# Optimization experiments

Measured on AMD Instinct MI355X. Metric: run time of the kernel, lower is better.

The kernel has to match this reference:

```python
import jax, jax.numpy as jnp
import numpy as np
from functools import partial

PAD, SOD = 1, 2
VOCAB, E, H = 32000, 512, 512
BSZ, DOCLEN, SENTLEN, SRCLEN = 8, 16, 40, 400
MAXPOS = 62  # max_target_positions + 2
NEG = -1e9


def setup_inputs() -> dict:
    key = jax.random.key(0)
    ks = jax.random.split(key, 16)
    s = 0.05  # weight scale for numerical sanity
    emb = jax.random.normal(ks[0], (VOCAB, E), jnp.float32) * 0.1
    emb = emb.at[PAD].set(0.0)
    spe = jax.random.normal(ks[1], (MAXPOS, E), jnp.float32) * 0.1
    spe = spe.at[PAD].set(0.0)
    return {
        'prev_output_tokens': jax.random.randint(ks[2], (BSZ, DOCLEN, SENTLEN), 0, VOCAB),
        'encoder_out0': jax.random.normal(ks[3], (BSZ, SRCLEN, H), jnp.float32),
        'encoder_out1': jax.random.normal(ks[4], (BSZ, SRCLEN, H), jnp.float32),
        'encoder_padding_mask': jnp.zeros((BSZ, SRCLEN), bool),
        'embed_tokens': emb,
        'sent_pos_emb': spe,
        'w_ih_doc': jax.random.normal(ks[5], (4 * H, E), jnp.float32) * s,
        'w_hh_doc': jax.random.normal(ks[6], (4 * H, H), jnp.float32) * s,
        'b_ih_doc': jnp.zeros((4 * H,), jnp.float32),
        'b_hh_doc': jnp.zeros((4 * H,), jnp.float32),
        'attn_q_doc': jax.random.normal(ks[7], (H, H), jnp.float32) * s,
        'attn_o_doc': jax.random.normal(ks[8], (H, 2 * H), jnp.float32) * s,
        'w_ih_w': jax.random.normal(ks[9], (4 * H, E), jnp.float32) * s,
        'w_hh_w': jax.random.normal(ks[10], (4 * H, H), jnp.float32) * s,
        'b_ih_w': jnp.zeros((4 * H,), jnp.float32),
        'b_hh_w': jnp.zeros((4 * H,), jnp.float32),
        'attn_q_w': jax.random.normal(ks[11], (H, H), jnp.float32) * s,
        'attn_o_w': jax.random.normal(ks[12], (H, 2 * H), jnp.float32) * s,
        'fc_out_w': jax.random.normal(ks[13], (VOCAB, H), jnp.float32) * s,
        'fc_out_b': jnp.zeros((VOCAB,), jnp.float32),
    }


def _lstm_cell(x, h, c, w_ih, w_hh, b_ih, b_hh):
    g = x @ w_ih.T + h @ w_hh.T + b_ih + b_hh
    i, f, gg, o = jnp.split(g, 4, axis=-1)
    c = jax.nn.sigmoid(f) * c + jax.nn.sigmoid(i) * jnp.tanh(gg)
    h = jax.nn.sigmoid(o) * jnp.tanh(c)
    return h, c


def _attend(h, src, mask, wq, wo):
    # fairseq-style additive-bilinear attention: score = <src, Wq h>
    q = h @ wq.T                                  # [b, d]
    s = jnp.einsum('bsd,bd->bs', src, q)          # [b, srclen]
    s = jnp.where(mask, NEG, s)
    p = jax.nn.softmax(s, axis=-1)
    ctx = jnp.einsum('bs,bsd->bd', p, src)
    out = jnp.tanh(jnp.concatenate([ctx, h], axis=-1) @ wo.T)
    return out, p


def reference(prev_output_tokens, encoder_out0, encoder_out1, encoder_padding_mask,
              embed_tokens, sent_pos_emb,
              w_ih_doc, w_hh_doc, b_ih_doc, b_hh_doc, attn_q_doc, attn_o_doc,
              w_ih_w, w_hh_w, b_ih_w, b_hh_w, attn_q_w, attn_o_w,
              fc_out_w, fc_out_b):
    bsz, doclen, sentlen = prev_output_tokens.shape
    srclen = encoder_out0.shape[1]

    # ---- document-level LSTM + attention loop (one step per sentence) ----
    h0 = encoder_out0.mean(axis=1)                 # src_summary_h0
    x0 = jnp.broadcast_to(embed_tokens[SOD], (bsz, E))

    def doc_step(carry, _):
        h, c, inp = carry
        h, c = _lstm_cell(inp, h, c, w_ih_doc, w_hh_doc, b_ih_doc, b_hh_doc)
        out, _p = _attend(h, encoder_out0, encoder_padding_mask, attn_q_doc, attn_o_doc)
        return (h, c, out), out

    (_, _, last_out), doc_outs = jax.lax.scan(doc_step, (h0, h0, x0), None, length=doclen)
    sent_states = doc_outs.transpose(1, 0, 2).reshape(bsz * doclen, H)

    # ---- sentence positions (make_sent_positions) ----
    nonempty = (prev_output_tokens != PAD).sum(axis=2) != 0     # [bsz, doclen]
    pos = jnp.where(nonempty, PAD + 1 + jnp.arange(doclen), 1)
    sp = sent_pos_emb[pos.reshape(bsz * doclen)]                # [B2, E]

    # ---- word-level decoder over flattened sentences ----
    B2 = bsz * doclen
    ys = prev_output_tokens.reshape(B2, sentlen)
    x_in = embed_tokens[ys] + sp[:, None, :]                    # [B2, S, E]
    enc_w = jnp.repeat(encoder_out1, doclen, axis=0)            # [B2, srclen, d]
    mask_w = jnp.repeat(encoder_padding_mask, doclen, axis=0)

    def word_step(carry, x_t):
        h, c = carry
        h, c = _lstm_cell(x_t, h, c, w_ih_w, w_hh_w, b_ih_w, b_hh_w)
        out, p = _attend(h, enc_w, mask_w, attn_q_w, attn_o_w)
        return (h, c), (out, p)

    (_, _), (w_outs, w_scores) = jax.lax.scan(
        word_step, (sent_states, sent_states), x_in.transpose(1, 0, 2))
    w_outs = w_outs.transpose(1, 0, 2)                          # [B2, S, H]
    word_atte_scores = w_scores.transpose(1, 0, 2)              # [B2, S, srclen]

    logits = jnp.einsum('bsh,vh->bsv', w_outs, fc_out_w) + fc_out_b
    dec_outs = logits.reshape(bsz, doclen * sentlen, VOCAB)

    attn_scores = jnp.zeros((bsz, doclen, srclen), dec_outs.dtype)  # zeros as in original
    return dec_outs, attn_scores, word_atte_scores, last_out
```

## Files before the change

### kernel.cpp

```cpp
#include <hip/hip_runtime.h>
#include <cstdint>

typedef unsigned short u16;
typedef unsigned int u32;
typedef __attribute__((ext_vector_type(8))) short bf16x8;
typedef __attribute__((ext_vector_type(8))) unsigned short u16x8;
typedef __attribute__((ext_vector_type(4))) float f32x4;

struct us4 { u16 a, b, c, d; };

__device__ __forceinline__ u16 f2bf(float f) {
    uint32_t u = __float_as_uint(f);
    uint32_t r = (u + 0x7FFFu + ((u >> 16) & 1u)) >> 16;
    return (u16)r;
}
__device__ __forceinline__ float bf2f(u16 h) { return __uint_as_float(((uint32_t)h) << 16); }
__device__ __forceinline__ float sigm(float x) { return 1.f / (1.f + expf(-x)); }
__device__ __forceinline__ float dot4(float4 a, float4 b) {
    return a.x * b.x + a.y * b.y + a.z * b.z + a.w * b.w;
}
__device__ __forceinline__ float wave_sum(float v) {
#pragma unroll
    for (int o = 32; o; o >>= 1) v += __shfl_down(v, o);
    return v;
}
__device__ __forceinline__ float wave_max(float v) {
#pragma unroll
    for (int o = 32; o; o >>= 1) v = fmaxf(v, __shfl_down(v, o));
    return v;
}

__device__ __forceinline__ void ast(u32* p, u32 v) {
    __hip_atomic_store(p, v, __ATOMIC_RELAXED, __HIP_MEMORY_SCOPE_AGENT);
}
__device__ __forceinline__ u32 ald(const u32* p) {
    return __hip_atomic_load(p, __ATOMIC_RELAXED, __HIP_MEMORY_SCOPE_AGENT);
}
__device__ __forceinline__ u32 packsplit(float v) {
    u16 h = f2bf(v);
    u16 l = f2bf(v - bf2f(h));
    return (u32)h | ((u32)l << 16);
}

template <int NBLK>
__device__ __forceinline__ void fbar(u32* flags, int me, u32 gen) {
    asm volatile("s_waitcnt vmcnt(0)" ::: "memory");
    __syncthreads();
    if (threadIdx.x == 0) ast(&flags[me * 32], gen);
    if (threadIdx.x < NBLK) {
        while (ald(&flags[threadIdx.x * 32]) < gen)
            __builtin_amdgcn_s_sleep(1);
    }
    __syncthreads();
    asm volatile("" ::: "memory");
}

template <bool SPLIT, int AMODE, int EPI, int XMAJ = 0>
__global__ __launch_bounds__(256) void gemm_bt(
    const u16* __restrict__ AH, const u16* __restrict__ AL, int lda, long strideA,
    const u16* __restrict__ BH, const u16* __restrict__ BL, int ldb, long strideB,
    float* __restrict__ C, u16* __restrict__ CH, u16* __restrict__ CL,
    int ldc, long strideC, const float* __restrict__ bias, int K)
{
    constexpr int TL = 40;
    constexpr int CHK = 128 * TL;
    __shared__ u16 sm[(SPLIT ? 4 : 2) * CHK];
    u16* sAH = sm;
    u16* sBH = sm + CHK;
    u16* sAL = SPLIT ? sm + 2 * CHK : sm;
    u16* sBL = SPLIT ? sm + 3 * CHK : sm;

    const int tid = threadIdx.x;
    const int lane = tid & 63, w = tid >> 6;
    const int wm = w >> 1, wn = w & 1;
    const int lane15 = lane & 15, q8 = (lane >> 4) << 3;
    const int n0 = (XMAJ ? blockIdx.y : blockIdx.x) * 128;
    const int m0 = (XMAJ ? blockIdx.x : blockIdx.y) * 128;
    const int z = blockIdx.z;

    const int r = tid >> 2, c8 = (tid & 3) * 8;

    long aoff[2], boff[2];
#pragma unroll
    for (int h2 = 0; h2 < 2; ++h2) {
        int row = r + (h2 << 6);
        if (AMODE == 0) {
            aoff[h2] = strideA * z + (long)(m0 + row) * lda + c8;
        } else {
            int m = m0 + row;
            int t = m % 40, dd = m / 40;
            aoff[h2] = ((long)(t + 1) * 128 + (z * 16 + dd)) * 512 + c8;
        }
        boff[h2] = strideB * z + (long)(n0 + row) * ldb + c8;
    }

    f32x4 acc[4][4] = {};

    for (int k0 = 0; k0 < K; k0 += 32) {
#pragma unroll
        for (int h2 = 0; h2 < 2; ++h2) {
            int row = r + (h2 << 6);
            int sidx = row * TL + c8;
            *(u16x8*)&sAH[sidx] = *(const u16x8*)&AH[aoff[h2] + k0];
            *(u16x8*)&sBH[sidx] = *(const u16x8*)&BH[boff[h2] + k0];
            if constexpr (SPLIT) {
                *(u16x8*)&sAL[sidx] = *(const u16x8*)&AL[aoff[h2] + k0];
                *(u16x8*)&sBL[sidx] = *(const u16x8*)&BL[boff[h2] + k0];
            }
        }
        __syncthreads();

        bf16x8 a[4], b[4], al[4], bl[4];
#pragma unroll
        for (int i = 0; i < 4; ++i) {
            a[i] = *(const bf16x8*)&sAH[(wm * 64 + i * 16 + lane15) * TL + q8];
            b[i] = *(const bf16x8*)&sBH[(wn * 64 + i * 16 + lane15) * TL + q8];
            if constexpr (SPLIT) {
                al[i] = *(const bf16x8*)&sAL[(wm * 64 + i * 16 + lane15) * TL + q8];
                bl[i] = *(const bf16x8*)&sBL[(wn * 64 + i * 16 + lane15) * TL + q8];
            }
        }
#pragma unroll
        for (int mt = 0; mt < 4; ++mt)
#pragma unroll
            for (int nt = 0; nt < 4; ++nt) {
                acc[mt][nt] = __builtin_amdgcn_mfma_f32_16x16x32_bf16(a[mt], b[nt], acc[mt][nt], 0, 0, 0);
                if constexpr (SPLIT) {
                    acc[mt][nt] = __builtin_amdgcn_mfma_f32_16x16x32_bf16(a[mt], bl[nt], acc[mt][nt], 0, 0, 0);
                    acc[mt][nt] = __builtin_amdgcn_mfma_f32_16x16x32_bf16(al[mt], b[nt], acc[mt][nt], 0, 0, 0);
                }
            }
        __syncthreads();
    }

#pragma unroll
    for (int mt = 0; mt < 4; ++mt)
#pragma unroll
        for (int nt = 0; nt < 4; ++nt)
#pragma unroll
            for (int i = 0; i < 4; ++i) {
                int row = m0 + wm * 64 + mt * 16 + ((lane >> 4) << 2) + i;
                int col = n0 + wn * 64 + nt * 16 + lane15;
                long off = strideC * z + (long)row * ldc + col;
                float v = acc[mt][nt][i];
                if constexpr (EPI == 0) {
                    C[off] = v;
                } else if constexpr (EPI == 1) {
                    C[off] = v + bias[col];
                } else if constexpr (EPI == 2) {
                    u16 h_ = f2bf(v);
                    CH[off] = h_;
                    CL[off] = f2bf(v - bf2f(h_));
                } else if constexpr (EPI == 3) {
                    CH[off] = f2bf(tanhf(v));
                } else {
                    CH[off] = f2bf(v);
                }
            }
}

__global__ __launch_bounds__(256) void gemm_head(
    const u16* __restrict__ enc1H, const u16* __restrict__ enc1L,
    const u16* __restrict__ wqTH,  const u16* __restrict__ wqTL,
    const u16* __restrict__ enc0H, const u16* __restrict__ enc0L,
    const u16* __restrict__ wqdTH, const u16* __restrict__ wqdTL,
    const u16* __restrict__ woCH,  const u16* __restrict__ woCL,
    const u16* __restrict__ xinH,  const u16* __restrict__ xinL,
    const u16* __restrict__ WihH,  const u16* __restrict__ WihL,
    u16* __restrict__ sq1H, u16* __restrict__ sq1L,
    float* __restrict__ E0q, float* __restrict__ E0o,
    float* __restrict__ xW, const float* __restrict__ biasc)
{
    constexpr int TL = 40;
    constexpr int CHK = 128 * TL;
    __shared__ u16 sm[4 * CHK];
    u16* sAH = sm;
    u16* sBH = sm + CHK;
    u16* sAL = sm + 2 * CHK;
    u16* sBL = sm + 3 * CHK;

    const int bid = blockIdx.x;
    const u16 *AH, *AL, *BH, *BL;
    int task, n0, m0, ldc;
    if (bid < 300) {
        task = bid / 100;
        int rr = bid % 100;
        n0 = (rr & 3) * 128; m0 = (rr >> 2) * 128; ldc = 512;
        if (task == 0)      { AH = enc1H; AL = enc1L; BH = wqTH;  BL = wqTL;  }
        else if (task == 1) { AH = enc0H; AL = enc0L; BH = wqdTH; BL = wqdTL; }
        else                { AH = enc0H; AL = enc0L; BH = woCH;  BL = woCL;  }
    } else {
        task = 3;
        int rr = bid - 300;
        n0 = (rr & 15) * 128; m0 = (rr >> 4) * 128; ldc = 2048;
        AH = xinH; AL = xinL; BH = WihH; BL = WihL;
    }

    const int tid = threadIdx.x;
    const int lane = tid & 63, w = tid >> 6;
    const int wm = w >> 1, wn = w & 1;
    const int lane15 = lane & 15, q8 = (lane >> 4) << 3;
    const int r = tid >> 2, c8 = (tid & 3) * 8;

    long aoff[2], boff[2];
#pragma unroll
    for (int h2 = 0; h2 < 2; ++h2) {
        int row = r + (h2 << 6);
        aoff[h2] = (long)(m0 + row) * 512 + c8;
        boff[h2] = (long)(n0 + row) * 512 + c8;
    }

    f32x4 acc[4][4] = {};
    for (int k0 = 0; k0 < 512; k0 += 32) {
#pragma unroll
        for (int h2 = 0; h2 < 2; ++h2) {
            int row = r + (h2 << 6);
            int sidx = row * TL + c8;
            *(u16x8*)&sAH[sidx] = *(const u16x8*)&AH[aoff[h2] + k0];
            *(u16x8*)&sBH[sidx] = *(const u16x8*)&BH[boff[h2] + k0];
            *(u16x8*)&sAL[sidx] = *(const u16x8*)&AL[aoff[h2] + k0];
            *(u16x8*)&sBL[sidx] = *(const u16x8*)&BL[boff[h2] + k0];
        }
        __syncthreads();
        bf16x8 a[4], b[4], al[4], bl[4];
#pragma unroll
        for (int i = 0; i < 4; ++i) {
            a[i]  = *(const bf16x8*)&sAH[(wm * 64 + i * 16 + lane15) * TL + q8];
            b[i]  = *(const bf16x8*)&sBH[(wn * 64 + i * 16 + lane15) * TL + q8];
            al[i] = *(const bf16x8*)&sAL[(wm * 64 + i * 16 + lane15) * TL + q8];
            bl[i] = *(const bf16x8*)&sBL[(wn * 64 + i * 16 + lane15) * TL + q8];
        }
#pragma unroll
        for (int mt = 0; mt < 4; ++mt)
#pragma unroll
            for (int nt = 0; nt < 4; ++nt) {
                acc[mt][nt] = __builtin_amdgcn_mfma_f32_16x16x32_bf16(a[mt],  b[nt],  acc[mt][nt], 0, 0, 0);
                acc[mt][nt] = __builtin_amdgcn_mfma_f32_16x16x32_bf16(a[mt],  bl[nt], acc[mt][nt], 0, 0, 0);
                acc[mt][nt] = __builtin_amdgcn_mfma_f32_16x16x32_bf16(al[mt], b[nt],  acc[mt][nt], 0, 0, 0);
            }
        __syncthreads();
    }

#pragma unroll
    for (int mt = 0; mt < 4; ++mt)
#pragma unroll
        for (int nt = 0; nt < 4; ++nt)
#pragma unroll
            for (int i = 0; i < 4; ++i) {
                int row = m0 + wm * 64 + mt * 16 + ((lane >> 4) << 2) + i;
                int col = n0 + wn * 64 + nt * 16 + lane15;
                long off = (long)row * ldc + col;
                float v = acc[mt][nt][i];
                if (task == 0) {
                    u16 h_ = f2bf(v);
                    sq1H[off] = h_;
                    sq1L[off] = f2bf(v - bf2f(h_));
                } else if (task == 1) {
                    E0q[off] = v;
                } else if (task == 2) {
                    E0o[off] = v;
                } else {
                    xW[off] = v + biasc[col];
                }
            }
}

#define GLOAD_LDS16(gsrc, ldst) \
    __builtin_amdgcn_global_load_lds((const __attribute__((address_space(1))) u32*)(gsrc), \
                                     (__attribute__((address_space(3))) u32*)(ldst), 16, 0, 0)

__global__ __launch_bounds__(256) void gemm_lds_bias(
    const u16* __restrict__ A, const u16* __restrict__ B,
    float* __restrict__ C, const float* __restrict__ bias, int ldc, int K)
{
    __shared__ u16 sA[128 * 32];
    __shared__ u16 sB[128 * 32];

    const int tid = threadIdx.x;
    const int lane = tid & 63, w = tid >> 6;
    const int wm = w >> 1, wn = w & 1;
    const int lane15 = lane & 15, q8 = (lane >> 4) << 3;
    const int m0 = blockIdx.x * 128;
    const int n0 = blockIdx.y * 128;

    const int srow = lane >> 2, schunk = (lane & 3) * 8;

    f32x4 acc[4][4] = {};

    for (int k0 = 0; k0 < K; k0 += 32) {
#pragma unroll
        for (int c = 0; c < 2; ++c) {
            int base_r = (w * 2 + c) * 16;
            const u16* ga = A + (long)(m0 + base_r + srow) * 512 + k0 + schunk;
            const u16* gb = B + (long)(n0 + base_r + srow) * 512 + k0 + schunk;
            GLOAD_LDS16(ga, &sA[base_r * 32]);
            GLOAD_LDS16(gb, &sB[base_r * 32]);
        }
        __syncthreads();

        bf16x8 a[4], b[4];
#pragma unroll
        for (int i = 0; i < 4; ++i) {
            a[i] = *(const bf16x8*)&sA[(wm * 64 + i * 16 + lane15) * 32 + q8];
            b[i] = *(const bf16x8*)&sB[(wn * 64 + i * 16 + lane15) * 32 + q8];
        }
#pragma unroll
        for (int mt = 0; mt < 4; ++mt)
#pragma unroll
            for (int nt = 0; nt < 4; ++nt)
                acc[mt][nt] = __builtin_amdgcn_mfma_f32_16x16x32_bf16(a[mt], b[nt], acc[mt][nt], 0, 0, 0);
        __syncthreads();
    }

#pragma unroll
    for (int mt = 0; mt < 4; ++mt)
#pragma unroll
        for (int nt = 0; nt < 4; ++nt)
#pragma unroll
            for (int i = 0; i < 4; ++i) {
                int row = m0 + wm * 64 + mt * 16 + ((lane >> 4) << 2) + i;
                int col = n0 + wn * 64 + nt * 16 + lane15;
                __builtin_nontemporal_store(acc[mt][nt][i] + bias[col], &C[(long)row * ldc + col]);
            }
}

__global__ __launch_bounds__(256) void doc_mega(
    const float* __restrict__ enc0, const float* __restrict__ E0q,
    const float* __restrict__ E0o, const unsigned char* __restrict__ mask,
    const float* __restrict__ emb,
    const u16* __restrict__ WpH, const u16* __restrict__ WpL,
    const float* __restrict__ biasd, const float* __restrict__ wo_d,
    u32* __restrict__ dxP, u32* __restrict__ hP0, u32* __restrict__ hP1,
    u32* __restrict__ dcP, u32* __restrict__ dscP,
    float* __restrict__ dsent, float* __restrict__ out_last, u32* bar)
{
    __shared__ u16 xhH[16 * 1032];
    __shared__ u16 xhL[16 * 1032];
    __shared__ float red4[4][16 * 17];
    __shared__ float aux2[512];
    __shared__ float sc_s[512];
    __shared__ float whoh_s[32];
    __shared__ float ctxp[8][32];
    __shared__ float rtmp[8];

    const int blk = blockIdx.x, tid = threadIdx.x;
    const int w = tid >> 6, lane = tid & 63;
    const int b_ = blk >> 4, s = blk & 15;
    const int lane15 = lane & 15, q8 = (lane >> 4) << 3;
    u32* fF = bar;
    u32* fG = bar + 4096 + b_ * 512;
    u32 genF = 0, genG = 0;

    for (int q = tid; q < 8 * 1032; q += 256) { xhH[8 * 1032 + q] = 0; xhL[8 * 1032 + q] = 0; }

    {
        int dd = tid & 31, part = tid >> 5;
        const float* p0 = enc0 + ((long)b_ * 400 + part * 50) * 512 + s * 32 + dd;
        float sm = 0.f;
#pragma unroll 10
        for (int j = 0; j < 50; ++j) { sm += *p0; p0 += 512; }
        ctxp[part][dd] = sm;
        __syncthreads();
        if (tid < 32) {
            float m = 0.f;
#pragma unroll
            for (int p = 0; p < 8; ++p) m += ctxp[p][tid];
            m *= (1.f / 400.f);
            int e = s * 32 + tid;
            ast(&hP0[b_ * 512 + e], packsplit(m));
            ast(&dcP[b_ * 512 + e], __float_as_uint(m));
            ast(&dxP[b_ * 512 + e], packsplit(emb[1024 + e]));
        }
    }
    fbar<128>(fF, blk, ++genF);

    const int eb_b = tid & 7, eb_u4 = tid >> 3, eb_u = blk * 4 + eb_u4;
    float dcr = 0.f;
    if (tid < 32) dcr = __uint_as_float(ald(&dcP[eb_b * 512 + eb_u]));

    const u16* bh_base = WpH + ((long)blk * 16 + lane15) * 1024 + (w << 8) + q8;
    const u16* bl_base = WpL + ((long)blk * 16 + lane15) * 1024 + (w << 8) + q8;
    const u16* ah_base = xhH + lane15 * 1032 + (w << 8) + q8;
    const u16* al_base = xhL + lane15 * 1032 + (w << 8) + q8;

    for (int t = 0; t < 16; ++t) {
        u32* hinP = (t & 1) ? hP1 : hP0;
        u32* houtP = (t & 1) ? hP0 : hP1;

#pragma unroll
        for (int half = 0; half < 2; ++half) {
            u32 px[8], ph[8];
#pragma unroll
            for (int j = 0; j < 8; ++j) {
                int q = half * 2048 + j * 256 + tid;
                px[j] = ald(&dxP[q]);
                ph[j] = ald(&hinP[q]);
            }
#pragma unroll
            for (int j = 0; j < 8; ++j) {
                int q = half * 2048 + j * 256 + tid;
                int o = (q >> 9) * 1032 + (q & 511);
                xhH[o] = (u16)px[j];           xhL[o] = (u16)(px[j] >> 16);
                xhH[o + 512] = (u16)ph[j];     xhL[o + 512] = (u16)(ph[j] >> 16);
            }
        }
        __syncthreads();

        f32x4 acc = {};
#pragma unroll
        for (int k0 = 0; k0 < 256; k0 += 32) {
            bf16x8 aH = *(const bf16x8*)&ah_base[k0];
            bf16x8 aL = *(const bf16x8*)&al_base[k0];
            bf16x8 bH = *(const bf16x8*)&bh_base[k0];
            bf16x8 bL = *(const bf16x8*)&bl_base[k0];
            acc = __builtin_amdgcn_mfma_f32_16x16x32_bf16(aH, bH, acc, 0, 0, 0);
            acc = __builtin_amdgcn_mfma_f32_16x16x32_bf16(aH, bL, acc, 0, 0, 0);
            acc = __builtin_amdgcn_mfma_f32_16x16x32_bf16(aL, bH, acc, 0, 0, 0);
        }
#pragma unroll
        for (int i = 0; i < 4; ++i)
            red4[w][((lane >> 4) * 4 + i) * 17 + lane15] = acc[i];
        __syncthreads();

        if (tid < 32) {
            float g4[4];
#pragma unroll
            for (int g = 0; g < 4; ++g)
                g4[g] = red4[0][eb_b * 17 + eb_u4 * 4 + g] + red4[1][eb_b * 17 + eb_u4 * 4 + g]
                      + red4[2][eb_b * 17 + eb_u4 * 4 + g] + red4[3][eb_b * 17 + eb_u4 * 4 + g];
            float gi = g4[0] + biasd[eb_u];
            float gf = g4[1] + biasd[512 + eb_u];
            float gg = g4[2] + biasd[1024 + eb_u];
            float go = g4[3] + biasd[1536 + eb_u];
            dcr = sigm(gf) * dcr + sigm(gi) * tanhf(gg);
            float hv = sigm(go) * tanhf(dcr);
            ast(&houtP[eb_b * 512 + eb_u], packsplit(hv));
        }
        fbar<128>(fF, blk, ++genF);

        {
            u32 p0 = ald(&houtP[b_ * 512 + tid]);
            u32 p1 = ald(&houtP[b_ * 512 + 256 + tid]);
            aux2[tid] = bf2f((u16)p0) + bf2f((u16)(p0 >> 16));
            aux2[256 + tid] = bf2f((u16)p1) + bf2f((u16)(p1 >> 16));
            __syncthreads();
            for (int jj = w; jj < 25; jj += 4) {
                int j = s * 25 + jj;
                const float4* er = (const float4*)(E0q + ((long)b_ * 400 + j) * 512) + lane * 2;
                const float4* hv = (const float4*)aux2 + lane * 2;
                float sv = dot4(er[0], hv[0]) + dot4(er[1], hv[1]);
                sv = wave_sum(sv);
                if (lane == 0)
                    ast(&dscP[b_ * 400 + j], __float_as_uint(mask[b_ * 400 + j] ? -1e9f : sv));
            }
#pragma unroll
            for (int r = 0; r < 8; ++r) {
                int d = s * 32 + w * 8 + r;
                const float4* wr = (const float4*)(wo_d + (long)d * 1024 + 512) + lane * 2;
                const float4* hv = (const float4*)aux2 + lane * 2;
                float sv = dot4(wr[0], hv[0]) + dot4(wr[1], hv[1]);
                sv = wave_sum(sv);
                if (lane == 0) whoh_s[w * 8 + r] = sv;
            }
        }
        fbar<16>(fG, s, ++genG);

        {
            float v0 = __uint_as_float(ald(&dscP[b_ * 400 + tid]));
            bool h1 = (tid + 256) < 400;
            float v1 = h1 ? __uint_as_float(ald(&dscP[b_ * 400 + tid + 256])) : -1e30f;
            float mx = wave_max(fmaxf(v0, v1));
            if (lane == 0) rtmp[w] = mx;
            __syncthreads();
            float M = fmaxf(fmaxf(rtmp[0], rtmp[1]), fmaxf(rtmp[2], rtmp[3]));
            float e0 = expf(v0 - M);
            float e1 = h1 ? expf(v1 - M) : 0.f;
            float sv = wave_sum(e0 + e1);
            if (lane == 0) rtmp[4 + w] = sv;
            __syncthreads();
            float inv = 1.f / (rtmp[4] + rtmp[5] + rtmp[6] + rtmp[7]);
            sc_s[tid] = e0 * inv;
            if (h1) sc_s[tid + 256] = e1 * inv;
            __syncthreads();
            int dd = tid & 31, part = tid >> 5;
            const float* eo = E0o + ((long)b_ * 400 + part * 50) * 512 + s * 32 + dd;
            float acc2 = 0.f;
#pragma unroll 10
            for (int j = 0; j < 50; ++j) { acc2 += sc_s[part * 50 + j] * (*eo); eo += 512; }
            ctxp[part][dd] = acc2;
            __syncthreads();
            if (tid < 32) {
                int d = s * 32 + tid;
                float o = whoh_s[tid];
#pragma unroll
                for (int p = 0; p < 8; ++p) o += ctxp[p][tid];
                float val = tanhf(o);
                ast(&dxP[b_ * 512 + d], packsplit(val));
                dsent[((b_ << 4) + t) * 512 + d] = val;
                if (t == 15) out_last[b_ * 512 + d] = val;
            }
        }
        fbar<128>(fF, blk, ++genF);
    }
}

__global__ __launch_bounds__(512) void word_mega(
    const float* __restrict__ sentS,
    u32* __restrict__ hAllP,
    u16* __restrict__ hAllH, u16* __restrict__ hAllL,
    const u16* __restrict__ WhhH, const u16* __restrict__ WhhL,
    const float* __restrict__ xW,
    u16* __restrict__ catB, u32* bar)
{
    __shared__ float red[8][4][256];
    const int tid = threadIdx.x, blk = blockIdx.x;
    const int b2t = blk >> 5;
    const int u0 = (blk & 31) << 4;
    u32* fG = bar + 8192 + b2t * 1024;
    u32 genG = 0;

    float wcr = 0.f;
    long cidx = 0;
    int my_b2 = 0, my_u = 0;
    if (tid < 256) {
        my_b2 = b2t * 16 + (tid >> 4);
        my_u = u0 + (tid & 15);
        cidx = (long)my_b2 * 512 + my_u;
        wcr = sentS[cidx];
        ast(&hAllP[cidx], packsplit(wcr));
    }
    fbar<32>(fG, blk & 31, ++genG);

    const int w = tid >> 6, lane = tid & 63;
    const int lane15 = lane & 15, q8 = (lane >> 4) << 3;
    const long arowE = (long)(b2t * 16 + lane15) * 512 + w * 64 + q8;
    long brow[4];
#pragma unroll
    for (int g = 0; g < 4; ++g)
        brow[g] = (long)(g * 512 + u0 + lane15) * 512 + w * 64 + q8;

    for (int t = 0; t < 40; ++t) {
        const u32* hP = hAllP + (long)t * 65536;

        u32 ph[16];
#pragma unroll
        for (int j = 0; j < 16; ++j)
            ph[j] = ald(&hP[arowE + (j >> 3) * 32 + (j & 7)]);

        float xw0 = 0.f, xw1 = 0.f, xw2 = 0.f, xw3 = 0.f;
        if (tid < 256) {
            const float* xr = xW + (long)t * 262144 + (long)my_b2 * 2048;
            xw0 = xr[my_u]; xw1 = xr[512 + my_u]; xw2 = xr[1024 + my_u]; xw3 = xr[1536 + my_u];
        }

        f32x4 acc[4] = {};
#pragma unroll
        for (int half = 0; half < 2; ++half) {
            int k0 = half * 32;
            bf16x8 aH, aL;
#pragma unroll
            for (int j = 0; j < 8; ++j) {
                u32 p = ph[half * 8 + j];
                aH[j] = (short)(p & 0xffffu);
                aL[j] = (short)(p >> 16);
            }
#pragma unroll
            for (int g = 0; g < 4; ++g) {
                bf16x8 bH = *(const bf16x8*)&WhhH[brow[g] + k0];
                bf16x8 bL = *(const bf16x8*)&WhhL[brow[g] + k0];
                acc[g] = __builtin_amdgcn_mfma_f32_16x16x32_bf16(aH, bH, acc[g], 0, 0, 0);
                acc[g] = __builtin_amdgcn_mfma_f32_16x16x32_bf16(aH, bL, acc[g], 0, 0, 0);
                acc[g] = __builtin_amdgcn_mfma_f32_16x16x32_bf16(aL, bH, acc[g], 0, 0, 0);
            }
        }
#pragma unroll
        for (int g = 0; g < 4; ++g)
#pragma unroll
            for (int i = 0; i < 4; ++i)
                red[w][g][((lane >> 4) * 4 + i) * 16 + lane15] = acc[g][i];
        __syncthreads();

        if (tid < 256) {
            float g4[4] = {0.f, 0.f, 0.f, 0.f};
#pragma unroll
            for (int ks = 0; ks < 8; ++ks)
#pragma unroll
                for (int g = 0; g < 4; ++g)
                    g4[g] += red[ks][g][tid];
            float gi = g4[0] + xw0;
            float gf = g4[1] + xw1;
            float gg = g4[2] + xw2;
            float go = g4[3] + xw3;
            wcr = sigm(gf) * wcr + sigm(gi) * tanhf(gg);
            float hv = sigm(go) * tanhf(wcr);
            u16 hh = f2bf(hv);
            u16 ll = f2bf(hv - bf2f(hh));
            long o = (long)(t + 1) * 65536 + cidx;
            ast(&hAllP[o], (u32)hh | ((u32)ll << 16));
            hAllH[o] = hh;
            hAllL[o] = ll;
            catB[((long)my_b2 * 40 + t) * 1024 + 512 + my_u] = hh;
        }
        fbar<32>(fG, blk & 31, ++genG);
    }
}

__device__ __forceinline__ void split1(const float* __restrict__ src,
                                       u16* __restrict__ H, u16* __restrict__ L, long i)
{
    float4 v = ((const float4*)src)[i];
    u16 h0 = f2bf(v.x), h1 = f2bf(v.y), h2 = f2bf(v.z), h3 = f2bf(v.w);
    ((us4*)H)[i] = {h0, h1, h2, h3};
    ((us4*)L)[i] = {f2bf(v.x - bf2f(h0)), f2bf(v.y - bf2f(h1)),
                    f2bf(v.z - bf2f(h2)), f2bf(v.w - bf2f(h3))};
}
__device__ __forceinline__ void wqT1(const float* __restrict__ wq,
                                     u16* __restrict__ H, u16* __restrict__ L, int idx)
{
    int e = idx >> 9, d = idx & 511;
    float v = wq[(long)d * 512 + e];
    u16 h = f2bf(v);
    H[idx] = h;
    L[idx] = f2bf(v - bf2f(h));
}

__global__ __launch_bounds__(256) void prep_all(
    const float* __restrict__ wih_w, const float* __restrict__ whh_w,
    const float* __restrict__ enc1, const float* __restrict__ enc0,
    const float* __restrict__ wq_w, const float* __restrict__ wq_d,
    const float* __restrict__ wo_w, const float* __restrict__ fcw,
    const int* __restrict__ toks, const float* __restrict__ emb,
    const float* __restrict__ spe,
    const float* __restrict__ bih_w, const float* __restrict__ bhh_w,
    const float* __restrict__ bih_d, const float* __restrict__ bhh_d,
    const float* __restrict__ wih_d, const float* __restrict__ whh_d,
    const float* __restrict__ wo_d,
    u16* __restrict__ WihH, u16* __restrict__ WihL,
    u16* __restrict__ WhhH, u16* __restrict__ WhhL,
    u16* __restrict__ enc1H, u16* __restrict__ enc1L,
    u16* __restrict__ enc0H, u16* __restrict__ enc0L,
    u16* __restrict__ wqTH, u16* __restrict__ wqTL,
    u16* __restrict__ wqdTH, u16* __restrict__ wqdTL,
    u16* __restrict__ woB, u16* __restrict__ fcwB, u16* __restrict__ enc1T,
    u16* __restrict__ xinH, u16* __restrict__ xinL,
    u16* __restrict__ woCH, u16* __restrict__ woCL,
    u16* __restrict__ WpH, u16* __restrict__ WpL,
    float* __restrict__ biasc, float* __restrict__ biasd,
    float* __restrict__ out_attn, u32* __restrict__ bar)
{
    int b = blockIdx.x;
    const int tid = threadIdx.x;

    if (b < 1024) { split1(wih_w, WihH, WihL, (long)b * 256 + tid); return; }
    b -= 1024;
    if (b < 1024) { split1(whh_w, WhhH, WhhL, (long)b * 256 + tid); return; }
    b -= 1024;
    if (b < 1600) { split1(enc1, enc1H, enc1L, (long)b * 256 + tid); return; }
    b -= 1600;
    if (b < 1600) { split1(enc0, enc0H, enc0L, (long)b * 256 + tid); return; }
    b -= 1600;
    if (b < 1024) { wqT1(wq_w, wqTH, wqTL, b * 256 + tid); return; }
    b -= 1024;
    if (b < 1024) { wqT1(wq_d, wqdTH, wqdTL, b * 256 + tid); return; }
    b -= 1024;
    if (b < 512) {
        long i = (long)b * 256 + tid;
        float4 v = ((const float4*)wo_w)[i];
        ((us4*)woB)[i] = {f2bf(v.x), f2bf(v.y), f2bf(v.z), f2bf(v.w)};
        return;
    }
    b -= 512;
    if (b < 16000) {
        long i = (long)b * 256 + tid;
        float4 v = ((const float4*)fcw)[i];
        ((us4*)fcwB)[i] = {f2bf(v.x), f2bf(v.y), f2bf(v.z), f2bf(v.w)};
        return;
    }
    b -= 16000;
    if (b < 6656) {
        long idx = (long)b * 256 + tid;
        int j = (int)(idx % 416);
        long be = idx / 416;
        int e = (int)(be % 512);
        int bb = (int)(be / 512);
        float v = (j < 400) ? enc1[((long)bb * 400 + j) * 512 + e] : 0.f;
        enc1T[idx] = f2bf(v);
        return;
    }
    b -= 6656;
    if (b < 1280) {
        int g = b * 256 + tid;
        int m = g >> 6, e0 = (g & 63) << 3;
        int t = m >> 7, b2 = m & 127;
        int ne = 0;
        for (int s = 0; s < 40; ++s) ne |= (toks[b2 * 40 + s] != 1);
        int pos = ne ? (2 + (b2 & 15)) : 1;
        const float* ep = emb + (long)toks[b2 * 40 + t] * 512 + e0;
        const float* sp = spe + (long)pos * 512 + e0;
        long o = (long)m * 512 + e0;
#pragma unroll
        for (int j = 0; j < 8; ++j) {
            float v = ep[j] + sp[j];
            u16 h = f2bf(v);
            xinH[o + j] = h;
            xinL[o + j] = f2bf(v - bf2f(h));
        }
        return;
    }
    b -= 1280;
    if (b < 1) {
        for (int i = tid; i < 2048; i += 256) {
            biasc[i] = bih_w[i] + bhh_w[i];
            biasd[i] = bih_d[i] + bhh_d[i];
        }
        return;
    }
    b -= 1;
    if (b < 200) {
        out_attn[b * 256 + tid] = 0.f;
        return;
    }
    b -= 200;
    if (b < 1024) {
        int i = b * 256 + tid;
        int d = i >> 9, e = i & 511;
        float v = wo_d[(long)d * 1024 + e];
        u16 h = f2bf(v);
        woCH[i] = h;
        woCL[i] = f2bf(v - bf2f(h));
        return;
    }
    b -= 1024;
    if (b < 1024) {
        long gidx = (long)b * 256 + tid;
        int r = (int)(gidx >> 7);
        int k8 = ((int)gidx & 127) * 8;
        int u = r >> 2, g = r & 3;
        long orow = (long)(g * 512 + u);
#pragma unroll
        for (int j = 0; j < 8; ++j) {
            int k = k8 + j;
            float v = (k < 512) ? wih_d[orow * 512 + k] : whh_d[orow * 512 + k - 512];
            u16 h = f2bf(v);
            WpH[(long)r * 1024 + k] = h;
            WpL[(long)r * 1024 + k] = f2bf(v - bf2f(h));
        }
        return;
    }
    b -= 1024;
    bar[b * 256 + tid] = 0;
}

__global__ __launch_bounds__(256) void word_softmax(
    const float* __restrict__ sc, const unsigned char* __restrict__ mask,
    float* __restrict__ pout, u16* __restrict__ pbf)
{
    const int r = blockIdx.x, tid = threadIdx.x;
    const int b = r / 640;
    const int wv = tid >> 6, lane = tid & 63;
    __shared__ float red[4];
    const int j1 = tid + 256;
    float v0 = sc[(long)r * 512 + tid];
    if (mask[b * 400 + tid]) v0 = -1e9f;
    float v1 = -1e30f;
    if (j1 < 400) {
        v1 = sc[(long)r * 512 + j1];
        if (mask[b * 400 + j1]) v1 = -1e9f;
    }
    float mv = wave_max(fmaxf(v0, v1));
    if (lane == 0) red[wv] = mv;
    __syncthreads();
    if (tid == 0) red[0] = fmaxf(fmaxf(red[0], red[1]), fmaxf(red[2], red[3]));
    __syncthreads();
    const float M = red[0];
    float e0 = expf(v0 - M);
    float e1 = (j1 < 400) ? expf(v1 - M) : 0.f;
    __syncthreads();
    float sv = wave_sum(e0 + e1);
    if (lane == 0) red[wv] = sv;
    __syncthreads();
    if (tid == 0) red[0] = red[0] + red[1] + red[2] + red[3];
    __syncthreads();
    const float inv = 1.f / red[0];
    float p0 = e0 * inv;
    pout[(long)r * 400 + tid] = p0;
    pbf[(long)r * 416 + tid] = f2bf(p0);
    if (j1 < 400) {
        float p1 = e1 * inv;
        pout[(long)r * 400 + j1] = p1;
        pbf[(long)r * 416 + j1] = f2bf(p1);
    } else if (j1 < 416) {
        pbf[(long)r * 416 + j1] = 0;
    }
}

extern "C" void kernel_launch(void* const* d_in, const int* in_sizes, int n_in,
                              void* d_out, int out_size, void* d_ws, size_t ws_size,
                              hipStream_t stream)
{
    (void)in_sizes; (void)n_in; (void)out_size; (void)ws_size;

    const int*   toks  = (const int*)  d_in[0];
    const float* enc0  = (const float*)d_in[1];
    const float* enc1  = (const float*)d_in[2];
    const unsigned char* mask = (const unsigned char*)d_in[3];
    const float* emb   = (const float*)d_in[4];
    const float* spe   = (const float*)d_in[5];
    const float* wih_d = (const float*)d_in[6];
    const float* whh_d = (const float*)d_in[7];
    const float* bih_d = (const float*)d_in[8];
    const float* bhh_d = (const float*)d_in[9];
    const float* wq_d  = (const float*)d_in[10];
    const float* wo_d  = (const float*)d_in[11];
    const float* wih_w = (const float*)d_in[12];
    const float* whh_w = (const float*)d_in[13];
    const float* bih_w = (const float*)d_in[14];
    const float* bhh_w = (const float*)d_in[15];
    const float* wq_w  = (const float*)d_in[16];
    const float* wo_w  = (const float*)d_in[17];
    const float* fcw   = (const float*)d_in[18];
    const float* fcb   = (const float*)d_in[19];

    float* out_dec  = (float*)d_out;
    float* out_attn = out_dec + 163840000L;
    float* out_watt = out_attn + 51200;
    float* out_last = out_watt + 2048000;

    char* wsp = (char*)d_ws;
    auto alloc = [&](size_t bytes) -> void* {
        void* p = wsp;
        wsp += (bytes + 255) & ~(size_t)255;
        return p;
    };

    float* xW    = (float*)alloc(40L * 128 * 2048 * 4);
    u32* hAllP   = (u32*)alloc(41L * 128 * 512 * 4);
    u16* hAllH   = (u16*)alloc(41L * 128 * 512 * 2);
    u16* hAllL   = (u16*)alloc(41L * 128 * 512 * 2);
    u16* xinH    = (u16*)alloc(5120L * 512 * 2);
    u16* xinL    = (u16*)alloc(5120L * 512 * 2);
    u16* WihH    = (u16*)alloc(2048L * 512 * 2);
    u16* WihL    = (u16*)alloc(2048L * 512 * 2);
    u16* WhhH    = (u16*)alloc(2048L * 512 * 2);
    u16* WhhL    = (u16*)alloc(2048L * 512 * 2);
    u16* wqTH    = (u16*)alloc(512L * 512 * 2);
    u16* wqTL    = (u16*)alloc(512L * 512 * 2);
    u16* wqdTH   = (u16*)alloc(512L * 512 * 2);
    u16* wqdTL   = (u16*)alloc(512L * 512 * 2);
    u16* enc1H   = (u16*)alloc(3200L * 512 * 2);
    u16* enc1L   = (u16*)alloc(3200L * 512 * 2);
    u16* enc0H   = (u16*)alloc(3200L * 512 * 2);
    u16* enc0L   = (u16*)alloc(3200L * 512 * 2);
    u16* sq1H    = (u16*)alloc(3328L * 512 * 2);
    u16* sq1L    = (u16*)alloc(3328L * 512 * 2);
    float* E0q   = (float*)alloc(3200L * 512 * 4);
    float* E0o   = (float*)alloc(3200L * 512 * 4);
    u16* woCH    = (u16*)alloc(512L * 512 * 2);
    u16* woCL    = (u16*)alloc(512L * 512 * 2);
    u16* WpH     = (u16*)alloc(2048L * 1024 * 2);
    u16* WpL     = (u16*)alloc(2048L * 1024 * 2);
    float* wsS   = (float*)alloc(5120L * 512 * 4);
    u16* Pbf     = (u16*)alloc(5120L * 416 * 2);
    u16* enc1T   = (u16*)alloc(8L * 512 * 416 * 2);
    u16* catB    = (u16*)alloc(5120L * 1024 * 2);
    u16* woB     = (u16*)alloc(512L * 1024 * 2);
    u16* Alog    = (u16*)alloc(5120L * 512 * 2);
    u16* fcwB    = (u16*)alloc(32000L * 512 * 2);
    float* biasc = (float*)alloc(2048 * 4);
    float* biasd = (float*)alloc(2048 * 4);
    u32* dxP     = (u32*)alloc(4096 * 4);
    u32* hP0     = (u32*)alloc(4096 * 4);
    u32* hP1     = (u32*)alloc(4096 * 4);
    u32* dcP     = (u32*)alloc(4096 * 4);
    u32* dscP    = (u32*)alloc(3200 * 4);
    float* dsent = (float*)alloc(128L * 512 * 4);
    u32* bar     = (u32*)alloc(16384 * 4);

    prep_all<<<dim3(34057), 256, 0, stream>>>(
        wih_w, whh_w, enc1, enc0, wq_w, wq_d, wo_w, fcw, toks, emb, spe,
        bih_w, bhh_w, bih_d, bhh_d, wih_d, whh_d, wo_d,
        WihH, WihL, WhhH, WhhL, enc1H, enc1L, enc0H, enc0L,
        wqTH, wqTL, wqdTH, wqdTL, woB, fcwB, enc1T, xinH, xinL,
        woCH, woCL, WpH, WpL, biasc, biasd, out_attn, bar);

    gemm_head<<<dim3(940), 256, 0, stream>>>(
        enc1H, enc1L, wqTH, wqTL, enc0H, enc0L, wqdTH, wqdTL,
        woCH, woCL, xinH, xinL, WihH, WihL,
        sq1H, sq1L, E0q, E0o, xW, biasc);

    doc_mega<<<dim3(128), 256, 0, stream>>>(
        enc0, E0q, E0o, mask, emb, WpH, WpL, biasd, wo_d,
        dxP, hP0, hP1, dcP, dscP, dsent, out_last, bar);

    word_mega<<<dim3(256), 512, 0, stream>>>(
        dsent, hAllP, hAllH, hAllL, WhhH, WhhL, xW, catB, bar);

    gemm_bt<true, 1, 0><<<dim3(4, 5, 8), 256, 0, stream>>>(
        hAllH, hAllL, 0, 0, sq1H, sq1L, 512, 204800L,
        wsS, nullptr, nullptr, 512, 327680L, nullptr, 512);

    word_softmax<<<dim3(5120), 256, 0, stream>>>(wsS, mask, out_watt, Pbf);

    gemm_bt<false, 0, 4><<<dim3(4, 5, 8), 256, 0, stream>>>(
        Pbf, nullptr, 416, 266240L, enc1T, nullptr, 416, 212992L,
        nullptr, catB, nullptr, 1024, 655360L, nullptr, 416);

    gemm_bt<false, 0, 3><<<dim3(4, 40, 1), 256, 0, stream>>>(
        catB, nullptr, 1024, 0, woB, nullptr, 1024, 0,
        nullptr, Alog, nullptr, 512, 0, nullptr, 1024);

    gemm_lds_bias<<<dim3(40, 250, 1), 256, 0, stream>>>(
        Alog, fcwB, out_dec, fcb, 32000, 512);
}
```

Baseline: 977.1 us.

## Overlap head GEMMs with doc recurrence and enlarge FC output GEMM tile

Splits the head GEMM so that only the doc-attention projections (tasks 1-2) run before the doc recurrence. The enc1 query projection and the input-weight GEMM now run as extra blocks inside the doc kernel, so they can use idle CUs while the 128 recurrence blocks spin on barriers. The final vocab GEMM moves to 256x128 tiles with 512 threads to improve B-tile reuse, and softmax probability stores become nontemporal. The risk is that co-scheduled GEMM blocks delay the persistent recurrence blocks, or that doc blocks fail to become co-resident, which could stall the grid barrier.

```diff
diff --git a/kernel.cpp b/kernel.cpp
--- a/kernel.cpp
+++ b/kernel.cpp
@@ -159,7 +159,8 @@
             }
 }
 
-__global__ __launch_bounds__(256) void gemm_head(
+__device__ __forceinline__ void run_head_gemm(
+    int bid, u16* __restrict__ smem,
     const u16* __restrict__ enc1H, const u16* __restrict__ enc1L,
     const u16* __restrict__ wqTH,  const u16* __restrict__ wqTL,
     const u16* __restrict__ enc0H, const u16* __restrict__ enc0L,
@@ -173,13 +174,11 @@
 {
     constexpr int TL = 40;
     constexpr int CHK = 128 * TL;
-    __shared__ u16 sm[4 * CHK];
-    u16* sAH = sm;
-    u16* sBH = sm + CHK;
-    u16* sAL = sm + 2 * CHK;
-    u16* sBL = sm + 3 * CHK;
-
-    const int bid = blockIdx.x;
+    u16* sAH = smem;
+    u16* sBH = smem + CHK;
+    u16* sAL = smem + 2 * CHK;
+    u16* sBL = smem + 3 * CHK;
+
     const u16 *AH, *AL, *BH, *BL;
     int task, n0, m0, ldc;
     if (bid < 300) {
@@ -265,22 +264,42 @@
             }
 }
 
+__global__ __launch_bounds__(256) void gemm_head_k(
+    int bid_off,
+    const u16* __restrict__ enc1H, const u16* __restrict__ enc1L,
+    const u16* __restrict__ wqTH,  const u16* __restrict__ wqTL,
+    const u16* __restrict__ enc0H, const u16* __restrict__ enc0L,
+    const u16* __restrict__ wqdTH, const u16* __restrict__ wqdTL,
+    const u16* __restrict__ woCH,  const u16* __restrict__ woCL,
+    const u16* __restrict__ xinH,  const u16* __restrict__ xinL,
+    const u16* __restrict__ WihH,  const u16* __restrict__ WihL,
+    u16* __restrict__ sq1H, u16* __restrict__ sq1L,
+    float* __restrict__ E0q, float* __restrict__ E0o,
+    float* __restrict__ xW, const float* __restrict__ biasc)
+{
+    __shared__ u16 sm[4 * 128 * 40];
+    run_head_gemm(blockIdx.x + bid_off, sm,
+                  enc1H, enc1L, wqTH, wqTL, enc0H, enc0L, wqdTH, wqdTL,
+                  woCH, woCL, xinH, xinL, WihH, WihL,
+                  sq1H, sq1L, E0q, E0o, xW, biasc);
+}
+
 #define GLOAD_LDS16(gsrc, ldst) \
     __builtin_amdgcn_global_load_lds((const __attribute__((address_space(1))) u32*)(gsrc), \
                                      (__attribute__((address_space(3))) u32*)(ldst), 16, 0, 0)
 
-__global__ __launch_bounds__(256) void gemm_lds_bias(
+__global__ __launch_bounds__(512) void gemm_lds_bias256(
     const u16* __restrict__ A, const u16* __restrict__ B,
     float* __restrict__ C, const float* __restrict__ bias, int ldc, int K)
 {
-    __shared__ u16 sA[128 * 32];
+    __shared__ u16 sA[256 * 32];
     __shared__ u16 sB[128 * 32];
 
     const int tid = threadIdx.x;
     const int lane = tid & 63, w = tid >> 6;
     const int wm = w >> 1, wn = w & 1;
     const int lane15 = lane & 15, q8 = (lane >> 4) << 3;
-    const int m0 = blockIdx.x * 128;
+    const int m0 = blockIdx.x * 256;
     const int n0 = blockIdx.y * 128;
 
     const int srow = lane >> 2, schunk = (lane & 3) * 8;
@@ -290,10 +309,13 @@
     for (int k0 = 0; k0 < K; k0 += 32) {
 #pragma unroll
         for (int c = 0; c < 2; ++c) {
-            int base_r = (w * 2 + c) * 16;
+            int base_r = w * 32 + c * 16;
             const u16* ga = A + (long)(m0 + base_r + srow) * 512 + k0 + schunk;
+            GLOAD_LDS16(ga, &sA[base_r * 32]);
+        }
+        {
+            int base_r = w * 16;
             const u16* gb = B + (long)(n0 + base_r + srow) * 512 + k0 + schunk;
-            GLOAD_LDS16(ga, &sA[base_r * 32]);
             GLOAD_LDS16(gb, &sB[base_r * 32]);
         }
         __syncthreads();
@@ -324,7 +346,7 @@
             }
 }
 
-__global__ __launch_bounds__(256) void doc_mega(
+__global__ __launch_bounds__(256) void doc_plus_gemm(
     const float* __restrict__ enc0, const float* __restrict__ E0q,
     const float* __restrict__ E0o, const unsigned char* __restrict__ mask,
     const float* __restrict__ emb,
@@ -332,16 +354,38 @@
     const float* __restrict__ biasd, const float* __restrict__ wo_d,
     u32* __restrict__ dxP, u32* __restrict__ hP0, u32* __restrict__ hP1,
     u32* __restrict__ dcP, u32* __restrict__ dscP,
-    float* __restrict__ dsent, float* __restrict__ out_last, u32* bar)
-{
-    __shared__ u16 xhH[16 * 1032];
-    __shared__ u16 xhL[16 * 1032];
-    __shared__ float red4[4][16 * 17];
-    __shared__ float aux2[512];
-    __shared__ float sc_s[512];
-    __shared__ float whoh_s[32];
-    __shared__ float ctxp[8][32];
-    __shared__ float rtmp[8];
+    float* __restrict__ dsent, float* __restrict__ out_last, u32* bar,
+    const u16* __restrict__ enc1H, const u16* __restrict__ enc1L,
+    const u16* __restrict__ wqTH,  const u16* __restrict__ wqTL,
+    const u16* __restrict__ enc0H, const u16* __restrict__ enc0L,
+    const u16* __restrict__ wqdTH, const u16* __restrict__ wqdTL,
+    const u16* __restrict__ woCH,  const u16* __restrict__ woCL,
+    const u16* __restrict__ xinH,  const u16* __restrict__ xinL,
+    const u16* __restrict__ WihH,  const u16* __restrict__ WihL,
+    u16* __restrict__ sq1H, u16* __restrict__ sq1L,
+    float* __restrict__ xW, const float* __restrict__ biasc)
+{
+    __shared__ __attribute__((aligned(16))) char SM[75776];
+
+    if (blockIdx.x >= 128) {
+        int g = blockIdx.x - 128;
+        int bid = (g < 100) ? g : g + 200;
+        run_head_gemm(bid, (u16*)SM,
+                      enc1H, enc1L, wqTH, wqTL, enc0H, enc0L, wqdTH, wqdTL,
+                      woCH, woCL, xinH, xinL, WihH, WihL,
+                      sq1H, sq1L, nullptr, nullptr, xW, biasc);
+        return;
+    }
+
+    u16* xhH = (u16*)SM;
+    u16* xhL = xhH + 16 * 1032;
+    float* fb = (float*)(SM + 66048);
+    float* red4 = fb;
+    float* aux2 = fb + 1088;
+    float* sc_s = fb + 1600;
+    float* whoh_s = fb + 2112;
+    float* ctxp = fb + 2144;
+    float* rtmp = fb + 2400;
 
     const int blk = blockIdx.x, tid = threadIdx.x;
     const int w = tid >> 6, lane = tid & 63;
@@ -359,12 +403,12 @@
         float sm = 0.f;
 #pragma unroll 10
         for (int j = 0; j < 50; ++j) { sm += *p0; p0 += 512; }
-        ctxp[part][dd] = sm;
+        ctxp[part * 32 + dd] = sm;
         __syncthreads();
         if (tid < 32) {
             float m = 0.f;
 #pragma unroll
-            for (int p = 0; p < 8; ++p) m += ctxp[p][tid];
+            for (int p = 0; p < 8; ++p) m += ctxp[p * 32 + tid];
             m *= (1.f / 400.f);
             int e = s * 32 + tid;
             ast(&hP0[b_ * 512 + e], packsplit(m));
@@ -419,15 +463,15 @@
         }
 #pragma unroll
         for (int i = 0; i < 4; ++i)
-            red4[w][((lane >> 4) * 4 + i) * 17 + lane15] = acc[i];
+            red4[w * 272 + ((lane >> 4) * 4 + i) * 17 + lane15] = acc[i];
         __syncthreads();
 
         if (tid < 32) {
             float g4[4];
 #pragma unroll
             for (int g = 0; g < 4; ++g)
-                g4[g] = red4[0][eb_b * 17 + eb_u4 * 4 + g] + red4[1][eb_b * 17 + eb_u4 * 4 + g]
-                      + red4[2][eb_b * 17 + eb_u4 * 4 + g] + red4[3][eb_b * 17 + eb_u4 * 4 + g];
+                g4[g] = red4[0 * 272 + eb_b * 17 + eb_u4 * 4 + g] + red4[1 * 272 + eb_b * 17 + eb_u4 * 4 + g]
+                      + red4[2 * 272 + eb_b * 17 + eb_u4 * 4 + g] + red4[3 * 272 + eb_b * 17 + eb_u4 * 4 + g];
             float gi = g4[0] + biasd[eb_u];
             float gf = g4[1] + biasd[512 + eb_u];
             float gg = g4[2] + biasd[1024 + eb_u];
@@ -487,13 +531,13 @@
             float acc2 = 0.f;
 #pragma unroll 10
             for (int j = 0; j < 50; ++j) { acc2 += sc_s[part * 50 + j] * (*eo); eo += 512; }
-            ctxp[part][dd] = acc2;
+            ctxp[part * 32 + dd] = acc2;
             __syncthreads();
             if (tid < 32) {
                 int d = s * 32 + tid;
                 float o = whoh_s[tid];
 #pragma unroll
-                for (int p = 0; p < 8; ++p) o += ctxp[p][tid];
+                for (int p = 0; p < 8; ++p) o += ctxp[p * 32 + tid];
                 float val = tanhf(o);
                 ast(&dxP[b_ * 512 + d], packsplit(val));
                 dsent[((b_ << 4) + t) * 512 + d] = val;
@@ -783,11 +827,11 @@
     __syncthreads();
     const float inv = 1.f / red[0];
     float p0 = e0 * inv;
-    pout[(long)r * 400 + tid] = p0;
+    __builtin_nontemporal_store(p0, &pout[(long)r * 400 + tid]);
     pbf[(long)r * 416 + tid] = f2bf(p0);
     if (j1 < 400) {
         float p1 = e1 * inv;
-        pout[(long)r * 400 + j1] = p1;
+        __builtin_nontemporal_store(p1, &pout[(long)r * 400 + j1]);
         pbf[(long)r * 416 + j1] = f2bf(p1);
     } else if (j1 < 416) {
         pbf[(long)r * 416 + j1] = 0;
@@ -883,14 +927,18 @@
         wqTH, wqTL, wqdTH, wqdTL, woB, fcwB, enc1T, xinH, xinL,
         woCH, woCL, WpH, WpL, biasc, biasd, out_attn, bar);
 
-    gemm_head<<<dim3(940), 256, 0, stream>>>(
+    gemm_head_k<<<dim3(200), 256, 0, stream>>>(
+        100,
         enc1H, enc1L, wqTH, wqTL, enc0H, enc0L, wqdTH, wqdTL,
         woCH, woCL, xinH, xinL, WihH, WihL,
         sq1H, sq1L, E0q, E0o, xW, biasc);
 
-    doc_mega<<<dim3(128), 256, 0, stream>>>(
+    doc_plus_gemm<<<dim3(868), 256, 0, stream>>>(
         enc0, E0q, E0o, mask, emb, WpH, WpL, biasd, wo_d,
-        dxP, hP0, hP1, dcP, dscP, dsent, out_last, bar);
+        dxP, hP0, hP1, dcP, dscP, dsent, out_last, bar,
+        enc1H, enc1L, wqTH, wqTL, enc0H, enc0L, wqdTH, wqdTL,
+        woCH, woCL, xinH, xinL, WihH, WihL,
+        sq1H, sq1L, xW, biasc);
 
     word_mega<<<dim3(256), 512, 0, stream>>>(
         dsent, hAllP, hAllH, hAllL, WhhH, WhhL, xW, catB, bar);
@@ -909,6 +957,6 @@
         catB, nullptr, 1024, 0, woB, nullptr, 1024, 0,
         nullptr, Alog, nullptr, 512, 0, nullptr, 1024);
 
-    gemm_lds_bias<<<dim3(40, 250, 1), 256, 0, stream>>>(
+    gemm_lds_bias256<<<dim3(20, 250, 1), 512, 0, stream>>>(
         Alog, fcwB, out_dec, fcb, 32000, 512);
 }
```

Result: faster. 931.5 us (median of 3 runs) (-4.7%).
